# Kernel tuning notes

Hardware: AMD Instinct MI355X
Metric: run time of the kernel (lower is better)

Reference implementation:

```python
import jax, jax.numpy as jnp
import numpy as np

EPS = 1e-12  # F.normalize eps
ALPHA = 1.0


def setup_inputs() -> dict:
    key = jax.random.key(0)
    k1, k2, k3, k4 = jax.random.split(key, 4)
    n_nodes, n_edges, d_in, d_out = 50000, 800000, 128, 128
    x = jax.random.normal(k1, (n_nodes, d_in), dtype=jnp.float32)
    W1 = jax.random.normal(k2, (d_out, d_in), dtype=jnp.float32) * (1.0 / np.sqrt(d_in))
    W2 = jax.random.normal(k3, (d_out, d_in), dtype=jnp.float32) * (1.0 / np.sqrt(d_in))
    edge_index = jax.random.randint(k4, (2, n_edges), 0, n_nodes, dtype=jnp.int64)
    return {"x": x, "W1": W1, "W2": W2, "edge_index": edge_index}


def reference(x, W1, W2, edge_index):
    n_nodes = x.shape[0]
    src, dst = edge_index[0], edge_index[1]
    # h_src = fc2(x)
    h = jnp.einsum('nd,od->no', x, W2)
    # out-degree normalization: h *= (deg_out + 1)^(-1/2)
    deg = jax.ops.segment_sum(jnp.ones(src.shape[0], dtype=x.dtype), src,
                              num_segments=n_nodes)
    h = h * ((deg + 1.0) ** -0.5)[:, None]
    # L2 normalize per node (F.normalize p=2 dim=1)
    nrm = jnp.sqrt(jnp.sum(h * h, axis=1, keepdims=True))
    h = h / jnp.maximum(nrm, EPS)
    # gather along edges, scatter-max to destinations
    msg = h[src]                                   # [E, d_out]
    agg = jax.ops.segment_max(msg, dst, num_segments=n_nodes)
    agg = jnp.where(jnp.isfinite(agg), agg, 0.0)   # empty segments -> 0 (torch_scatter semantics)
    # alpha * fc1(x) + aggregated messages
    return ALPHA * jnp.einsum('nd,od->no', x, W1) + agg
```

## Files before the change

### kernel.cpp

```cpp
#include <hip/hip_runtime.h>
#include <stdint.h>

#define N_NODES 50000
#define N_EDGES 800000
#define D 128
#define CAP 64
#define LDK 136
#define NBLK 391
#define NT_FILL (NBLK * 512)

typedef __attribute__((ext_vector_type(8))) short short8;
typedef __attribute__((ext_vector_type(4))) float f32x4;
typedef __attribute__((ext_vector_type(4))) unsigned short ush4;

__device__ __forceinline__ unsigned short f2bf(float f) {
    uint32_t u = __float_as_uint(f);
    u += 0x7FFFu + ((u >> 16) & 1u);
    return (unsigned short)(u >> 16);
}

__global__ __launch_bounds__(512) void gemm_fill(const float* __restrict__ x,
                                                 const float* __restrict__ W1,
                                                 const float* __restrict__ W2,
                                                 const int* __restrict__ ei,
                                                 float* __restrict__ out,
                                                 unsigned short* __restrict__ hbf,
                                                 int* __restrict__ cnt,
                                                 unsigned short* __restrict__ bucket)
{
    __shared__ unsigned short wsm[256][LDK];
    __shared__ unsigned short xs[128][LDK];

    const int t    = threadIdx.x;
    const int row0 = blockIdx.x * 128;
    const int gid  = blockIdx.x * 512 + t;

    int es[4], ed[4];
    #pragma unroll
    for (int k = 0; k < 4; ++k) {
        int e = gid + k * NT_FILL;
        bool v = (e < N_EDGES);
        es[k] = v ? ei[e] : 0;
        ed[k] = v ? ei[N_EDGES + e] : -1;
    }

    #pragma unroll
    for (int it = 0; it < 16; ++it) {
        int idx = it * 512 + t;
        int n = idx >> 5, c4 = idx & 31;
        const float* Wp = (n < 128) ? (W1 + (size_t)n * D) : (W2 + (size_t)(n - 128) * D);
        float4 v = *(const float4*)(Wp + c4 * 4);
        ush4 p; p[0] = f2bf(v.x); p[1] = f2bf(v.y); p[2] = f2bf(v.z); p[3] = f2bf(v.w);
        *(ush4*)&wsm[n][c4 * 4] = p;
    }
    #pragma unroll
    for (int it = 0; it < 8; ++it) {
        int idx = it * 512 + t;
        int r = idx >> 5, c4 = idx & 31;
        int gr = row0 + r;
        float4 v = make_float4(0.f, 0.f, 0.f, 0.f);
        if (gr < N_NODES) v = *(const float4*)(x + (size_t)gr * D + c4 * 4);
        ush4 p; p[0] = f2bf(v.x); p[1] = f2bf(v.y); p[2] = f2bf(v.z); p[3] = f2bf(v.w);
        *(ush4*)&xs[r][c4 * 4] = p;
    }
    __syncthreads();

    int ep[4];
    #pragma unroll
    for (int k = 0; k < 4; ++k)
        ep[k] = (ed[k] >= 0) ? atomicAdd(&cnt[ed[k]], 1) : CAP;

    const int wave = t >> 6;
    const int lane = t & 63;
    const int g    = lane >> 4;
    const int ln   = lane & 15;

    short8 afrag[4];
    #pragma unroll
    for (int ks = 0; ks < 4; ++ks)
        afrag[ks] = *(const short8*)&xs[wave * 16 + ln][ks * 32 + g * 8];

    f32x4 acc1[8], acc2[8];
    #pragma unroll
    for (int ct = 0; ct < 8; ++ct) {
        f32x4 a1 = {0.f, 0.f, 0.f, 0.f}, a2 = {0.f, 0.f, 0.f, 0.f};
        #pragma unroll
        for (int ks = 0; ks < 4; ++ks) {
            short8 b1 = *(const short8*)&wsm[      ct * 16 + ln][ks * 32 + g * 8];
            short8 b2 = *(const short8*)&wsm[128 + ct * 16 + ln][ks * 32 + g * 8];
            a1 = __builtin_amdgcn_mfma_f32_16x16x32_bf16(afrag[ks], b1, a1, 0, 0, 0);
            a2 = __builtin_amdgcn_mfma_f32_16x16x32_bf16(afrag[ks], b2, a2, 0, 0, 0);
        }
        acc1[ct] = a1; acc2[ct] = a2;
    }

    float ss[4] = {0.f, 0.f, 0.f, 0.f};
    #pragma unroll
    for (int ct = 0; ct < 8; ++ct)
        #pragma unroll
        for (int r = 0; r < 4; ++r)
            ss[r] = fmaf(acc2[ct][r], acc2[ct][r], ss[r]);
    #pragma unroll
    for (int r = 0; r < 4; ++r)
        #pragma unroll
        for (int o = 1; o < 16; o <<= 1)
            ss[r] += __shfl_xor(ss[r], o, 64);
    float scale[4];
    #pragma unroll
    for (int r = 0; r < 4; ++r)
        scale[r] = 1.0f / fmaxf(sqrtf(ss[r]), 1e-12f);

    #pragma unroll
    for (int r = 0; r < 4; ++r) {
        int grow = row0 + wave * 16 + g * 4 + r;
        if (grow < N_NODES) {
            #pragma unroll
            for (int ct = 0; ct < 8; ++ct) {
                out[(size_t)grow * D + ct * 16 + ln] = acc1[ct][r];
                hbf[(size_t)grow * D + ct * 16 + ln] = f2bf(acc2[ct][r] * scale[r]);
            }
        }
    }

    #pragma unroll
    for (int k = 0; k < 4; ++k)
        if (ed[k] >= 0 && ep[k] < CAP)
            bucket[ed[k] * CAP + ep[k]] = (unsigned short)es[k];
}

__global__ __launch_bounds__(256) void gather_max(const unsigned short* __restrict__ hbf,
                                                  const int* __restrict__ cnt,
                                                  const unsigned short* __restrict__ bucket,
                                                  float* __restrict__ out)
{
    int wid  = (blockIdx.x * 256 + threadIdx.x) >> 6;
    int lane = threadIdx.x & 63;
    if (wid >= N_NODES) return;
    int deg = cnt[wid];
    deg = (deg > CAP) ? CAP : deg;
    if (deg == 0) return;

    const uint32_t* h32 = (const uint32_t*)hbf;
    int sl = (lane < deg) ? (int)bucket[wid * CAP + lane] : 0;

    float mx = -INFINITY, my = -INFINITY;
    int j = 0;
    for (; j + 8 <= deg; j += 8) {
        uint32_t u[8];
        #pragma unroll
        for (int q = 0; q < 8; ++q) {
            int s = __shfl(sl, j + q, 64);
            u[q] = h32[(size_t)s * 64 + lane];
        }
        #pragma unroll
        for (int q = 0; q < 8; ++q) {
            mx = fmaxf(mx, __uint_as_float(u[q] << 16));
            my = fmaxf(my, __uint_as_float(u[q] & 0xFFFF0000u));
        }
    }
    for (; j < deg; ++j) {
        int s = __shfl(sl, j, 64);
        uint32_t u = h32[(size_t)s * 64 + lane];
        mx = fmaxf(mx, __uint_as_float(u << 16));
        my = fmaxf(my, __uint_as_float(u & 0xFFFF0000u));
    }

    float2* o2 = (float2*)out;
    float2 o = o2[(size_t)wid * 64 + lane];
    o.x += mx; o.y += my;
    o2[(size_t)wid * 64 + lane] = o;
}

extern "C" void kernel_launch(void* const* d_in, const int* in_sizes, int n_in,
                              void* d_out, int out_size, void* d_ws, size_t ws_size,
                              hipStream_t stream)
{
    const float* x  = (const float*)d_in[0];
    const float* W1 = (const float*)d_in[1];
    const float* W2 = (const float*)d_in[2];
    const int*   ei = (const int*)d_in[3];
    float* out = (float*)d_out;

    char* ws = (char*)d_ws;
    unsigned short* hbf    = (unsigned short*)ws;
    int*            cnt    = (int*)(ws + (size_t)N_NODES * D * 2);
    unsigned short* bucket = (unsigned short*)(ws + (size_t)N_NODES * D * 2
                                                  + (size_t)N_NODES * 4);

    hipMemsetAsync(cnt, 0, (size_t)N_NODES * 4, stream);
    gemm_fill<<<NBLK, 512, 0, stream>>>(x, W1, W2, ei, out, hbf, cnt, bucket);
    gather_max<<<(N_NODES * 64 + 255) / 256, 256, 0, stream>>>(hbf, cnt, bucket, out);
}
```

Baseline: 162.2 us.

## Pre-convert weights to bf16 once and drop LDS staging in GEMM kernel

Adds a small kernel that zeroes the degree counters and converts W1/W2 to bf16 once, replacing the memset and the per-block weight conversion. The GEMM kernel now uses 256-thread blocks of 64 rows, loads x directly from global into MFMA fragments and reads bf16 weights straight from global/L2, with no shared memory or barrier. This is meant to cut the redundant per-block weight conversion and LDS traffic and to raise occupancy. The gather loop is also unrolled to 16 loads, with a bounded remainder. The cost is repeated uncoalesced global reads of the weights per wave and one extra launch.

```diff
diff --git a/kernel.cpp b/kernel.cpp
--- a/kernel.cpp
+++ b/kernel.cpp
@@ -5,13 +5,11 @@
 #define N_EDGES 800000
 #define D 128
 #define CAP 64
-#define LDK 136
-#define NBLK 391
-#define NT_FILL (NBLK * 512)
+#define NBLK 782
+#define NT2 (NBLK * 256)
 
 typedef __attribute__((ext_vector_type(8))) short short8;
 typedef __attribute__((ext_vector_type(4))) float f32x4;
-typedef __attribute__((ext_vector_type(4))) unsigned short ush4;
 
 __device__ __forceinline__ unsigned short f2bf(float f) {
     uint32_t u = __float_as_uint(f);
@@ -19,53 +17,43 @@
     return (unsigned short)(u >> 16);
 }
 
-__global__ __launch_bounds__(512) void gemm_fill(const float* __restrict__ x,
-                                                 const float* __restrict__ W1,
+__global__ __launch_bounds__(256) void convert_w(const float* __restrict__ W1,
                                                  const float* __restrict__ W2,
+                                                 unsigned short* __restrict__ wbf,
+                                                 int* __restrict__ cnt)
+{
+    int gid = blockIdx.x * 256 + threadIdx.x;
+    if (gid < N_NODES) cnt[gid] = 0;
+    if (gid < 8192) {
+        const float* src = (gid < 4096) ? W1 : W2;
+        int i = (gid < 4096) ? gid : gid - 4096;
+        float4 v = ((const float4*)src)[i];
+        unsigned short p0 = f2bf(v.x), p1 = f2bf(v.y), p2 = f2bf(v.z), p3 = f2bf(v.w);
+        uint32_t lo = (uint32_t)p0 | ((uint32_t)p1 << 16);
+        uint32_t hi = (uint32_t)p2 | ((uint32_t)p3 << 16);
+        ((uint2*)wbf)[gid] = make_uint2(lo, hi);
+    }
+}
+
+__global__ __launch_bounds__(256) void gemm_fill(const float* __restrict__ x,
+                                                 const unsigned short* __restrict__ wbf,
                                                  const int* __restrict__ ei,
                                                  float* __restrict__ out,
                                                  unsigned short* __restrict__ hbf,
                                                  int* __restrict__ cnt,
                                                  unsigned short* __restrict__ bucket)
 {
-    __shared__ unsigned short wsm[256][LDK];
-    __shared__ unsigned short xs[128][LDK];
-
-    const int t    = threadIdx.x;
-    const int row0 = blockIdx.x * 128;
-    const int gid  = blockIdx.x * 512 + t;
-
-    int es[4], ed[4];
+    const int t   = threadIdx.x;
+    const int gid = blockIdx.x * 256 + t;
+
+    int es[4], ed[4], ep[4];
     #pragma unroll
     for (int k = 0; k < 4; ++k) {
-        int e = gid + k * NT_FILL;
+        int e = gid + k * NT2;
         bool v = (e < N_EDGES);
         es[k] = v ? ei[e] : 0;
         ed[k] = v ? ei[N_EDGES + e] : -1;
     }
-
-    #pragma unroll
-    for (int it = 0; it < 16; ++it) {
-        int idx = it * 512 + t;
-        int n = idx >> 5, c4 = idx & 31;
-        const float* Wp = (n < 128) ? (W1 + (size_t)n * D) : (W2 + (size_t)(n - 128) * D);
-        float4 v = *(const float4*)(Wp + c4 * 4);
-        ush4 p; p[0] = f2bf(v.x); p[1] = f2bf(v.y); p[2] = f2bf(v.z); p[3] = f2bf(v.w);
-        *(ush4*)&wsm[n][c4 * 4] = p;
-    }
-    #pragma unroll
-    for (int it = 0; it < 8; ++it) {
-        int idx = it * 512 + t;
-        int r = idx >> 5, c4 = idx & 31;
-        int gr = row0 + r;
-        float4 v = make_float4(0.f, 0.f, 0.f, 0.f);
-        if (gr < N_NODES) v = *(const float4*)(x + (size_t)gr * D + c4 * 4);
-        ush4 p; p[0] = f2bf(v.x); p[1] = f2bf(v.y); p[2] = f2bf(v.z); p[3] = f2bf(v.w);
-        *(ush4*)&xs[r][c4 * 4] = p;
-    }
-    __syncthreads();
-
-    int ep[4];
     #pragma unroll
     for (int k = 0; k < 4; ++k)
         ep[k] = (ed[k] >= 0) ? atomicAdd(&cnt[ed[k]], 1) : CAP;
@@ -74,20 +62,34 @@
     const int lane = t & 63;
     const int g    = lane >> 4;
     const int ln   = lane & 15;
-
+    const int rowbase = blockIdx.x * 64 + wave * 16;
+
+    int arow  = rowbase + ln;
+    int arowc = (arow < N_NODES) ? arow : (N_NODES - 1);
     short8 afrag[4];
     #pragma unroll
-    for (int ks = 0; ks < 4; ++ks)
-        afrag[ks] = *(const short8*)&xs[wave * 16 + ln][ks * 32 + g * 8];
-
+    for (int ks = 0; ks < 4; ++ks) {
+        const float* ap = x + (size_t)arowc * D + ks * 32 + g * 8;
+        float4 v0 = *(const float4*)ap;
+        float4 v1 = *(const float4*)(ap + 4);
+        short8 a;
+        a[0] = (short)f2bf(v0.x); a[1] = (short)f2bf(v0.y);
+        a[2] = (short)f2bf(v0.z); a[3] = (short)f2bf(v0.w);
+        a[4] = (short)f2bf(v1.x); a[5] = (short)f2bf(v1.y);
+        a[6] = (short)f2bf(v1.z); a[7] = (short)f2bf(v1.w);
+        afrag[ks] = a;
+    }
+
+    const unsigned short* w1bf = wbf;
+    const unsigned short* w2bf = wbf + 16384;
     f32x4 acc1[8], acc2[8];
     #pragma unroll
     for (int ct = 0; ct < 8; ++ct) {
         f32x4 a1 = {0.f, 0.f, 0.f, 0.f}, a2 = {0.f, 0.f, 0.f, 0.f};
         #pragma unroll
         for (int ks = 0; ks < 4; ++ks) {
-            short8 b1 = *(const short8*)&wsm[      ct * 16 + ln][ks * 32 + g * 8];
-            short8 b2 = *(const short8*)&wsm[128 + ct * 16 + ln][ks * 32 + g * 8];
+            short8 b1 = *(const short8*)&w1bf[(ct * 16 + ln) * D + ks * 32 + g * 8];
+            short8 b2 = *(const short8*)&w2bf[(ct * 16 + ln) * D + ks * 32 + g * 8];
             a1 = __builtin_amdgcn_mfma_f32_16x16x32_bf16(afrag[ks], b1, a1, 0, 0, 0);
             a2 = __builtin_amdgcn_mfma_f32_16x16x32_bf16(afrag[ks], b2, a2, 0, 0, 0);
         }
@@ -112,7 +114,7 @@
 
     #pragma unroll
     for (int r = 0; r < 4; ++r) {
-        int grow = row0 + wave * 16 + g * 4 + r;
+        int grow = rowbase + g * 4 + r;
         if (grow < N_NODES) {
             #pragma unroll
             for (int ct = 0; ct < 8; ++ct) {
@@ -145,24 +147,30 @@
 
     float mx = -INFINITY, my = -INFINITY;
     int j = 0;
-    for (; j + 8 <= deg; j += 8) {
-        uint32_t u[8];
-        #pragma unroll
-        for (int q = 0; q < 8; ++q) {
+    for (; j + 16 <= deg; j += 16) {
+        uint32_t u[16];
+        #pragma unroll
+        for (int q = 0; q < 16; ++q) {
             int s = __shfl(sl, j + q, 64);
             u[q] = h32[(size_t)s * 64 + lane];
         }
         #pragma unroll
-        for (int q = 0; q < 8; ++q) {
+        for (int q = 0; q < 16; ++q) {
             mx = fmaxf(mx, __uint_as_float(u[q] << 16));
             my = fmaxf(my, __uint_as_float(u[q] & 0xFFFF0000u));
         }
     }
-    for (; j < deg; ++j) {
-        int s = __shfl(sl, j, 64);
-        uint32_t u = h32[(size_t)s * 64 + lane];
-        mx = fmaxf(mx, __uint_as_float(u << 16));
-        my = fmaxf(my, __uint_as_float(u & 0xFFFF0000u));
+    if (j < deg) {
+        int rem = deg - j;
+        uint32_t u[15];
+        for (int q = 0; q < rem; ++q) {
+            int s = __shfl(sl, j + q, 64);
+            u[q] = h32[(size_t)s * 64 + lane];
+        }
+        for (int q = 0; q < rem; ++q) {
+            mx = fmaxf(mx, __uint_as_float(u[q] << 16));
+            my = fmaxf(my, __uint_as_float(u[q] & 0xFFFF0000u));
+        }
     }
 
     float2* o2 = (float2*)out;
@@ -186,8 +194,11 @@
     int*            cnt    = (int*)(ws + (size_t)N_NODES * D * 2);
     unsigned short* bucket = (unsigned short*)(ws + (size_t)N_NODES * D * 2
                                                   + (size_t)N_NODES * 4);
-
-    hipMemsetAsync(cnt, 0, (size_t)N_NODES * 4, stream);
-    gemm_fill<<<NBLK, 512, 0, stream>>>(x, W1, W2, ei, out, hbf, cnt, bucket);
+    unsigned short* wbf    = (unsigned short*)(ws + (size_t)N_NODES * D * 2
+                                                  + (size_t)N_NODES * 4
+                                                  + (size_t)N_NODES * CAP * 2);
+
+    convert_w<<<196, 256, 0, stream>>>(W1, W2, wbf, cnt);
+    gemm_fill<<<NBLK, 256, 0, stream>>>(x, wbf, ei, out, hbf, cnt, bucket);
     gather_max<<<(N_NODES * 64 + 255) / 256, 256, 0, stream>>>(hbf, cnt, bucket, out);
 }
```

After: 193.5 us. +19.3%, slower.
